# Kernel optimization log

Measured on AMD Instinct MI355X. Metric: run time of the kernel, lower is better.

## Reference

```python
import jax, jax.numpy as jnp
import numpy as np

TAU = 2.0
DECAY = float(np.exp(-1.0 / TAU))
THRESH = 1.0  # base_threshold; adaptive update only happens in training mode
LN_EPS = 1e-5
B, S, V, D, L = 16, 256, 32000, 512, 4  # d_state must equal d_model (see shape_source)

@jax.custom_vjp
def atan_spike(x):
    # spikingjelly surrogate.ATan: heaviside fwd, atan surrogate bwd (alpha=2)
    return (x >= 0).astype(x.dtype)

def _atan_fwd(x):
    return atan_spike(x), x

def _atan_bwd(x, g):
    alpha = 2.0
    s = (jnp.pi / 2.0) * alpha * x
    return (g * (alpha / 2.0) / (1.0 + s * s),)

atan_spike.defvjp(_atan_fwd, _atan_bwd)

def lif_step(mem, x):
    mem = mem * DECAY + x
    spike = atan_spike(mem - THRESH)
    mem = mem * (1.0 - jax.lax.stop_gradient(spike))  # reset uses spike.detach()
    return mem, spike

def layer_norm(x, g, b):
    m = jnp.mean(x, axis=-1, keepdims=True)
    v = jnp.mean(jnp.square(x - m), axis=-1, keepdims=True)
    return (x - m) / jnp.sqrt(v + LN_EPS) * g + b

def setup_inputs():
    key = jax.random.key(0)
    ks = jax.random.split(key, 8)
    s = 0.02
    return {
        'input_ids': jax.random.randint(ks[0], (B, S), 0, V),
        'embedding': jax.random.normal(ks[1], (V, D), jnp.float32) * s,
        'enc_W': jax.random.normal(ks[2], (D, D), jnp.float32) * s,
        'enc_b': jnp.zeros((D,), jnp.float32),
        'gen_W': jax.random.normal(ks[3], (L, D, D), jnp.float32) * s,
        'gen_b': jnp.zeros((L, D), jnp.float32),
        'inf_W': jax.random.normal(ks[4], (L, D, D), jnp.float32) * s,
        'inf_b': jnp.zeros((L, D), jnp.float32),
        'err_g': jnp.ones((L, D), jnp.float32),
        'err_b': jnp.zeros((L, D), jnp.float32),
        'st_g': jnp.ones((L, D), jnp.float32),
        'st_b': jnp.zeros((L, D), jnp.float32),
        'out_W': jax.random.normal(ks[5], (V, D), jnp.float32) * s,
        'out_b': jnp.zeros((V,), jnp.float32),
    }

def reference(input_ids, embedding, enc_W, enc_b, gen_W, gen_b, inf_W, inf_b, err_g, err_b, st_g, st_b, out_W, out_b):
    tok = embedding[input_ids]              # [B,S,D]
    xs = jnp.swapaxes(tok, 0, 1)            # [S,B,D] scan over time

    def pc_layer(j, gm, im, bottom_up, top_down):
        # PredictiveCodingLayer.forward (LIF mems gm/im are persistent state)
        gm, pred = lif_step(gm, top_down @ gen_W[j].T + gen_b[j])
        err = layer_norm(jax.nn.relu(bottom_up - pred), err_g[j], err_b[j])
        im, su = lif_step(im, err @ inf_W[j].T + inf_b[j])
        new_state = layer_norm(top_down + su, st_g[j], st_b[j])
        return gm, im, new_state, err, pred

    def step(carry, emb_t):
        enc_mem, gen_mem, inf_mem, states, spk, memp = carry
        enc_mem, bu = lif_step(enc_mem, emb_t @ enc_W.T + enc_b)
        # bottom-up pass
        for j in range(L):
            gm, im, st, err, _ = pc_layer(j, gen_mem[j], inf_mem[j], bu, states[j])
            gen_mem = gen_mem.at[j].set(gm)
            inf_mem = inf_mem.at[j].set(im)
            states = states.at[j].set(st)
            bu = jax.nn.relu(st)
            spk = spk + err.mean()
            memp = memp + jnp.abs(im).mean()
        # top-down generative pass (same layers called again: mems keep evolving)
        td = states[L - 1]
        zb = jnp.zeros_like(bu)
        for j in reversed(range(L)):
            gm, im, _, _, pred = pc_layer(j, gen_mem[j], inf_mem[j], zb, td)
            gen_mem = gen_mem.at[j].set(gm)
            inf_mem = inf_mem.at[j].set(im)
            td = pred
        logits = td @ out_W.T + out_b
        return (enc_mem, gen_mem, inf_mem, states, spk, memp), logits

    init = (jnp.zeros((B, D), jnp.float32), jnp.zeros((L, B, D), jnp.float32),
            jnp.zeros((L, B, D), jnp.float32), jnp.zeros((L, B, D), jnp.float32),
            jnp.float32(0.0), jnp.float32(0.0))
    (_, _, _, _, spk, memp), logits_sb = jax.lax.scan(step, init, xs)
    final_logits = jnp.swapaxes(logits_sb, 0, 1)  # [B,S,V]
    return final_logits, spk / S, memp / S
```

## Files before the change

kernel.cpp:

```cpp
#include <hip/hip_runtime.h>
#include <math.h>

#define S_ 256
#define B_ 16
#define D_ 512
#define V_ 32000
#define L_ 4
#define DEC_ 0.6065306597126334f

typedef short v8s __attribute__((ext_vector_type(8)));
typedef float v4f __attribute__((ext_vector_type(4)));

static __device__ __forceinline__ short f2bf(float f){
  union { float f; unsigned u; } v; v.f = f;
  unsigned r = (v.u + 0x7FFFu + ((v.u >> 16) & 1u)) >> 16;
  return (short)(unsigned short)r;
}

__global__ __launch_bounds__(64) void k_cj(const float* __restrict__ inf_W,
                                           const float* __restrict__ inf_b,
                                           const float* __restrict__ err_b,
                                           float* __restrict__ cvec,
                                           unsigned* __restrict__ counts,
                                           unsigned* __restrict__ bunz,
                                           float* __restrict__ accum){
  int g = blockIdx.x * 64 + threadIdx.x;
  #pragma unroll
  for (int i = 0; i < 2; ++i){
    counts[g + i*2048] = 0u;
    bunz[g + i*2048] = 0u;
  }
  if (g < 2) accum[g] = 0.0f;

  int j = blockIdx.x >> 3;
  int dp = (blockIdx.x & 7) * 64 + threadIdx.x;
  const float* row = inf_W + ((size_t)j * D_ + dp) * D_;
  const float* eb = err_b + j * D_;
  float acc = inf_b[j * D_ + dp];
  for (int d = 0; d < D_; d += 8){
    float4 w0 = *(const float4*)(row + d);
    float4 w1 = *(const float4*)(row + d + 4);
    float4 e0 = *(const float4*)(eb + d);
    float4 e1 = *(const float4*)(eb + d + 4);
    acc += e0.x*w0.x + e0.y*w0.y + e0.z*w0.z + e0.w*w0.w;
    acc += e1.x*w1.x + e1.y*w1.y + e1.z*w1.z + e1.w*w1.w;
  }
  cvec[j * D_ + dp] = acc;
}

__global__ __launch_bounds__(256) void k_gemm_enc(const int* __restrict__ ids,
                                                  const float* __restrict__ emb,
                                                  const float* __restrict__ encW,
                                                  const float* __restrict__ encb,
                                                  float* __restrict__ X){
  __shared__ __align__(16) short As[64*40];
  __shared__ __align__(16) short Bs[64*40];
  __shared__ int ids_s[64];
  const int t = threadIdx.x;
  const int bm = blockIdx.x, bn = blockIdx.y;
  if (t < 64){
    int mg = bm*64 + t;
    int s = mg >> 4, b = mg & 15;
    ids_s[t] = ids[b * S_ + s];
  }
  __syncthreads();
  const int arow = t >> 2;
  const int kc = (t & 3) * 8;
  const int wave = t >> 6;
  const int l = t & 63;
  const int lm = l & 15;
  const int q = l >> 4;
  v4f acc[4] = {};
  for (int k0 = 0; k0 < D_; k0 += 32){
    const float* asrc = emb + (size_t)ids_s[arow] * D_ + k0 + kc;
    float4 a0 = *(const float4*)asrc;
    float4 a1 = *(const float4*)(asrc + 4);
    const float* bsrc = encW + (size_t)(bn*64 + arow) * D_ + k0 + kc;
    float4 b0 = *(const float4*)bsrc;
    float4 b1 = *(const float4*)(bsrc + 4);
    v8s av, bv;
    av[0]=f2bf(a0.x); av[1]=f2bf(a0.y); av[2]=f2bf(a0.z); av[3]=f2bf(a0.w);
    av[4]=f2bf(a1.x); av[5]=f2bf(a1.y); av[6]=f2bf(a1.z); av[7]=f2bf(a1.w);
    bv[0]=f2bf(b0.x); bv[1]=f2bf(b0.y); bv[2]=f2bf(b0.z); bv[3]=f2bf(b0.w);
    bv[4]=f2bf(b1.x); bv[5]=f2bf(b1.y); bv[6]=f2bf(b1.z); bv[7]=f2bf(b1.w);
    *(v8s*)&As[arow*40 + kc] = av;
    *(v8s*)&Bs[arow*40 + kc] = bv;
    __syncthreads();
    v8s af = *(const v8s*)&As[(wave*16 + lm)*40 + q*8];
    #pragma unroll
    for (int n = 0; n < 4; ++n){
      v8s bf = *(const v8s*)&Bs[(n*16 + lm)*40 + q*8];
      acc[n] = __builtin_amdgcn_mfma_f32_16x16x32_bf16(af, bf, acc[n], 0, 0, 0);
    }
    __syncthreads();
  }
  #pragma unroll
  for (int n = 0; n < 4; ++n){
    #pragma unroll
    for (int i = 0; i < 4; ++i){
      int mloc = wave*16 + q*4 + i;
      int nloc = n*16 + lm;
      int r  = bm*64 + mloc;
      int nn = bn*64 + nloc;
      X[(size_t)r * D_ + nn] = acc[n][i] + encb[nn];
    }
  }
}

__global__ __launch_bounds__(64) void k_scan(const float* __restrict__ X,
                                             unsigned char* __restrict__ bu,
                                             unsigned* __restrict__ bunz){
  int g = blockIdx.x * 64 + threadIdx.x;
  int b = g >> 9;
  float mem = 0.0f;
  for (int s0 = 0; s0 < S_; s0 += 8){
    float x[8];
    #pragma unroll
    for (int i = 0; i < 8; ++i) x[i] = X[(size_t)(s0 + i) * (B_*D_) + g];
    #pragma unroll
    for (int i = 0; i < 8; ++i){
      mem = mem * DEC_ + x[i];
      float sp = (mem >= 1.0f) ? 1.0f : 0.0f;
      mem *= (1.0f - sp);
      bu[(size_t)(s0 + i) * (B_*D_) + g] = (unsigned char)sp;
      if (sp != 0.0f) atomicOr(&bunz[(s0 + i) * B_ + b], 1u);
    }
  }
}

__device__ __forceinline__ float wave_sum(float x){
  #pragma unroll
  for (int o = 32; o > 0; o >>= 1) x += __shfl_xor(x, o);
  return x;
}

__device__ void wave_matvec(const float* __restrict__ W, const float* __restrict__ bias,
                            const float x[8], float y[8], float* xs, int l){
  __syncthreads();
  #pragma unroll
  for (int i = 0; i < 8; ++i) xs[l + 64*i] = x[i];
  __syncthreads();
  #pragma unroll
  for (int i = 0; i < 8; ++i){
    int dp = l + 64*i;
    const float* row = W + (size_t)dp * D_;
    float acc = bias[dp];
    for (int d = 0; d < D_; d += 4){
      float4 w = *(const float4*)(row + d);
      acc += xs[d]*w.x + xs[d+1]*w.y + xs[d+2]*w.z + xs[d+3]*w.w;
    }
    y[i] = acc;
  }
}

__device__ void wave_ln(const float e[8], const float* __restrict__ g,
                        const float* __restrict__ bb, float out[8], int l){
  float s = 0.f;
  #pragma unroll
  for (int i = 0; i < 8; ++i) s += e[i];
  float m = wave_sum(s) * (1.0f/512.0f);
  float s2 = 0.f;
  #pragma unroll
  for (int i = 0; i < 8; ++i){ float d = e[i] - m; s2 += d*d; }
  float var = wave_sum(s2) * (1.0f/512.0f);
  float inv = 1.0f / sqrtf(var + 1e-5f);
  #pragma unroll
  for (int i = 0; i < 8; ++i){
    int d = l + 64*i;
    out[i] = (e[i] - m) * inv * g[d] + bb[d];
  }
}

__global__ __launch_bounds__(64) void k_sim(
    const float* __restrict__ gen_W, const float* __restrict__ gen_b,
    const float* __restrict__ inf_W, const float* __restrict__ inf_b,
    const float* __restrict__ err_g, const float* __restrict__ err_b,
    const float* __restrict__ st_g, const float* __restrict__ st_b,
    const unsigned char* __restrict__ bu8, const unsigned* __restrict__ bunz,
    const float* __restrict__ cvec,
    unsigned* __restrict__ counts, unsigned short* __restrict__ idxb,
    float* __restrict__ accum)
{
  const int b = blockIdx.x, l = threadIdx.x;
  __shared__ float xs[D_];
  __shared__ unsigned scnt;
  float st[4][8], gm[4][8], im[4][8];
  #pragma unroll
  for (int j = 0; j < 4; ++j)
    #pragma unroll
    for (int i = 0; i < 8; ++i){ st[j][i]=0.f; gm[j][i]=0.f; im[j][i]=0.f; }

  bool okz = true;
  #pragma unroll
  for (int j = 0; j < 4; ++j)
    #pragma unroll
    for (int i = 0; i < 8; ++i){
      int d = j*512 + l + 64*i;
      okz = okz && (gen_b[d]==0.f) && (inf_b[d]==0.f) && (err_b[d]==0.f) && (st_b[d]==0.f);
    }
  const bool bias_zero = (__all((int)okz) != 0);

  unsigned long long fl[4];
  #pragma unroll
  for (int w = 0; w < 4; ++w){
    unsigned v = bunz[(w*64 + l) * B_ + b];
    fl[w] = __ballot(v != 0u);
  }

  bool state_zero = true;
  float spk_acc = 0.f, memp_acc = 0.f;

  for (int t = 0; t < S_; ++t){
    bool nz = ((fl[t >> 6] >> (t & 63)) & 1ull) != 0ull;
    if (state_zero && bias_zero && !nz) continue;
    state_zero = false;

    float bu[8];
    #pragma unroll
    for (int i = 0; i < 8; ++i) bu[i] = (float)bu8[(size_t)(t*B_ + b)*D_ + l + 64*i];

    #pragma unroll
    for (int j = 0; j < 4; ++j){
      float y[8];
      wave_matvec(gen_W + (size_t)j*D_*D_, gen_b + j*D_, st[j], y, xs, l);
      float pred[8];
      #pragma unroll
      for (int i = 0; i < 8; ++i){
        gm[j][i] = gm[j][i]*DEC_ + y[i];
        pred[i] = (gm[j][i] >= 1.0f) ? 1.0f : 0.0f;
        gm[j][i] *= (1.0f - pred[i]);
      }
      float e[8];
      #pragma unroll
      for (int i = 0; i < 8; ++i){ float v = bu[i] - pred[i]; e[i] = v > 0.f ? v : 0.f; }
      float eo[8];
      wave_ln(e, err_g + j*D_, err_b + j*D_, eo, l);
      #pragma unroll
      for (int i = 0; i < 8; ++i) spk_acc += eo[i];
      float y2[8];
      wave_matvec(inf_W + (size_t)j*D_*D_, inf_b + j*D_, eo, y2, xs, l);
      float su[8];
      #pragma unroll
      for (int i = 0; i < 8; ++i){
        im[j][i] = im[j][i]*DEC_ + y2[i];
        su[i] = (im[j][i] >= 1.0f) ? 1.0f : 0.0f;
        im[j][i] *= (1.0f - su[i]);
        memp_acc += fabsf(im[j][i]);
      }
      float tmp[8];
      #pragma unroll
      for (int i = 0; i < 8; ++i) tmp[i] = st[j][i] + su[i];
      wave_ln(tmp, st_g + j*D_, st_b + j*D_, st[j], l);
      #pragma unroll
      for (int i = 0; i < 8; ++i) bu[i] = st[j][i] > 0.f ? st[j][i] : 0.f;
    }

    float td[8];
    #pragma unroll
    for (int i = 0; i < 8; ++i) td[i] = st[3][i];
    #pragma unroll
    for (int j = 3; j >= 0; --j){
      float y[8];
      wave_matvec(gen_W + (size_t)j*D_*D_, gen_b + j*D_, td, y, xs, l);
      #pragma unroll
      for (int i = 0; i < 8; ++i){
        gm[j][i] = gm[j][i]*DEC_ + y[i];
        float p = (gm[j][i] >= 1.0f) ? 1.0f : 0.0f;
        gm[j][i] *= (1.0f - p);
        td[i] = p;
      }
      #pragma unroll
      for (int i = 0; i < 8; ++i){
        float c = cvec[j*D_ + l + 64*i];
        im[j][i] = im[j][i]*DEC_ + c;
        float ss = (im[j][i] >= 1.0f) ? 1.0f : 0.0f;
        im[j][i] *= (1.0f - ss);
      }
    }

    if (l == 0) scnt = 0u;
    __syncthreads();
    unsigned base = (unsigned)(t*B_ + b) * D_;
    #pragma unroll
    for (int i = 0; i < 8; ++i){
      if (td[i] != 0.f){
        unsigned pos = atomicAdd(&scnt, 1u);
        idxb[base + pos] = (unsigned short)(l + 64*i);
      }
    }
    __syncthreads();
    if (l == 0) counts[t*B_ + b] = scnt;
  }
  spk_acc = wave_sum(spk_acc);
  memp_acc = wave_sum(memp_acc);
  if (l == 0){
    atomicAdd(&accum[0], spk_acc);
    atomicAdd(&accum[1], memp_acc);
  }
}

__global__ __launch_bounds__(256) void k_logits(const unsigned* __restrict__ counts,
                                                const unsigned short* __restrict__ idxb,
                                                const float* __restrict__ outW,
                                                const float* __restrict__ outb,
                                                const float* __restrict__ accum,
                                                float* __restrict__ out){
  __shared__ unsigned short sidx[D_];
  int bs = blockIdx.x;
  int b = bs >> 8, s = bs & 255;
  if (bs == 0 && threadIdx.x == 0){
    const float inv = 1.0f / (float)(B_ * D_ * S_);
    out[(size_t)B_ * S_ * V_ + 0] = accum[0] * inv;
    out[(size_t)B_ * S_ * V_ + 1] = accum[1] * inv;
  }
  unsigned k = counts[s * B_ + b];
  const float4* ob4 = (const float4*)outb;
  float4* o4 = (float4*)(out + (size_t)bs * V_);
  if (k == 0){
    #pragma unroll 4
    for (int v4 = threadIdx.x; v4 < V_/4; v4 += 256) o4[v4] = ob4[v4];
  } else {
    unsigned base = (unsigned)(s * B_ + b) * D_;
    for (unsigned i = threadIdx.x; i < k; i += 256) sidx[i] = idxb[base + i];
    __syncthreads();
    for (int v4 = threadIdx.x; v4 < V_/4; v4 += 256){
      float4 a = ob4[v4];
      int v = v4 * 4;
      for (unsigned i = 0; i < k; ++i){
        int d = sidx[i];
        a.x += outW[(size_t)(v+0)*D_ + d];
        a.y += outW[(size_t)(v+1)*D_ + d];
        a.z += outW[(size_t)(v+2)*D_ + d];
        a.w += outW[(size_t)(v+3)*D_ + d];
      }
      o4[v4] = a;
    }
  }
}

extern "C" void kernel_launch(void* const* d_in, const int* in_sizes, int n_in,
                              void* d_out, int out_size, void* d_ws, size_t ws_size,
                              hipStream_t stream){
  (void)in_sizes; (void)n_in; (void)out_size; (void)ws_size;
  const int*   input_ids = (const int*)d_in[0];
  const float* embedding = (const float*)d_in[1];
  const float* enc_W = (const float*)d_in[2];
  const float* enc_b = (const float*)d_in[3];
  const float* gen_W = (const float*)d_in[4];
  const float* gen_b = (const float*)d_in[5];
  const float* inf_W = (const float*)d_in[6];
  const float* inf_b = (const float*)d_in[7];
  const float* err_g = (const float*)d_in[8];
  const float* err_b = (const float*)d_in[9];
  const float* st_g  = (const float*)d_in[10];
  const float* st_b  = (const float*)d_in[11];
  const float* out_W = (const float*)d_in[12];
  const float* out_b = (const float*)d_in[13];
  float* out = (float*)d_out;
  char* ws = (char*)d_ws;

  float*          X      = (float*)(ws + 0);
  unsigned char*  bu     = (unsigned char*)(ws + 8388608);
  unsigned short* idxb   = (unsigned short*)(ws + 10485760);
  unsigned*       counts = (unsigned*)(ws + 14680064);
  unsigned*       bunz   = (unsigned*)(ws + 14696448);
  float*          cvec   = (float*)(ws + 14712832);
  float*          accum  = (float*)(ws + 14721024);

  hipLaunchKernelGGL(k_cj, dim3(32), dim3(64), 0, stream,
                     inf_W, inf_b, err_b, cvec, counts, bunz, accum);
  hipLaunchKernelGGL(k_gemm_enc, dim3(64, 8), dim3(256), 0, stream,
                     input_ids, embedding, enc_W, enc_b, X);
  hipLaunchKernelGGL(k_scan, dim3(128), dim3(64), 0, stream, X, bu, bunz);
  hipLaunchKernelGGL(k_sim, dim3(16), dim3(64), 0, stream,
                     gen_W, gen_b, inf_W, inf_b, err_g, err_b, st_g, st_b,
                     bu, bunz, cvec, counts, idxb, accum);
  hipLaunchKernelGGL(k_logits, dim3(4096), dim3(256), 0, stream,
                     counts, idxb, out_W, out_b, accum, out);
}
```

Baseline: 710.9 us.

## Fold prep kernel into encoder/scan and retile logits with nontemporal stores

```diff
diff --git a/kernel.cpp b/kernel.cpp
--- a/kernel.cpp
+++ b/kernel.cpp
@@ -17,47 +17,25 @@
   return (short)(unsigned short)r;
 }
 
-__global__ __launch_bounds__(64) void k_cj(const float* __restrict__ inf_W,
-                                           const float* __restrict__ inf_b,
-                                           const float* __restrict__ err_b,
-                                           float* __restrict__ cvec,
-                                           unsigned* __restrict__ counts,
-                                           unsigned* __restrict__ bunz,
-                                           float* __restrict__ accum){
-  int g = blockIdx.x * 64 + threadIdx.x;
-  #pragma unroll
-  for (int i = 0; i < 2; ++i){
-    counts[g + i*2048] = 0u;
-    bunz[g + i*2048] = 0u;
-  }
-  if (g < 2) accum[g] = 0.0f;
-
-  int j = blockIdx.x >> 3;
-  int dp = (blockIdx.x & 7) * 64 + threadIdx.x;
-  const float* row = inf_W + ((size_t)j * D_ + dp) * D_;
-  const float* eb = err_b + j * D_;
-  float acc = inf_b[j * D_ + dp];
-  for (int d = 0; d < D_; d += 8){
-    float4 w0 = *(const float4*)(row + d);
-    float4 w1 = *(const float4*)(row + d + 4);
-    float4 e0 = *(const float4*)(eb + d);
-    float4 e1 = *(const float4*)(eb + d + 4);
-    acc += e0.x*w0.x + e0.y*w0.y + e0.z*w0.z + e0.w*w0.w;
-    acc += e1.x*w1.x + e1.y*w1.y + e1.z*w1.z + e1.w*w1.w;
-  }
-  cvec[j * D_ + dp] = acc;
-}
-
 __global__ __launch_bounds__(256) void k_gemm_enc(const int* __restrict__ ids,
                                                   const float* __restrict__ emb,
                                                   const float* __restrict__ encW,
                                                   const float* __restrict__ encb,
-                                                  float* __restrict__ X){
+                                                  float* __restrict__ X,
+                                                  unsigned* __restrict__ counts,
+                                                  unsigned* __restrict__ bunz,
+                                                  float* __restrict__ accum){
   __shared__ __align__(16) short As[64*40];
   __shared__ __align__(16) short Bs[64*40];
   __shared__ int ids_s[64];
   const int t = threadIdx.x;
   const int bm = blockIdx.x, bn = blockIdx.y;
+  if (bn == 0 && bm < 16){
+    int g = bm*256 + t;
+    counts[g] = 0u;
+    bunz[g] = 0u;
+    if (g < 2) accum[g] = 0.0f;
+  }
   if (t < 64){
     int mg = bm*64 + t;
     int s = mg >> 4, b = mg & 15;
@@ -109,8 +87,31 @@
 
 __global__ __launch_bounds__(64) void k_scan(const float* __restrict__ X,
                                              unsigned char* __restrict__ bu,
-                                             unsigned* __restrict__ bunz){
-  int g = blockIdx.x * 64 + threadIdx.x;
+                                             unsigned* __restrict__ bunz,
+                                             const float* __restrict__ inf_W,
+                                             const float* __restrict__ inf_b,
+                                             const float* __restrict__ err_b,
+                                             float* __restrict__ cvec){
+  int bx = blockIdx.x;
+  if (bx >= 128){
+    int r = bx - 128;
+    int j = r >> 3;
+    int dp = (r & 7) * 64 + threadIdx.x;
+    const float* row = inf_W + ((size_t)j * D_ + dp) * D_;
+    const float* eb = err_b + j * D_;
+    float acc = inf_b[j * D_ + dp];
+    for (int d = 0; d < D_; d += 8){
+      float4 w0 = *(const float4*)(row + d);
+      float4 w1 = *(const float4*)(row + d + 4);
+      float4 e0 = *(const float4*)(eb + d);
+      float4 e1 = *(const float4*)(eb + d + 4);
+      acc += e0.x*w0.x + e0.y*w0.y + e0.z*w0.z + e0.w*w0.w;
+      acc += e1.x*w1.x + e1.y*w1.y + e1.z*w1.z + e1.w*w1.w;
+    }
+    cvec[j * D_ + dp] = acc;
+    return;
+  }
+  int g = bx * 64 + threadIdx.x;
   int b = g >> 9;
   float mem = 0.0f;
   for (int s0 = 0; s0 < S_; s0 += 8){
@@ -299,41 +300,57 @@
   }
 }
 
-__global__ __launch_bounds__(256) void k_logits(const unsigned* __restrict__ counts,
-                                                const unsigned short* __restrict__ idxb,
-                                                const float* __restrict__ outW,
-                                                const float* __restrict__ outb,
-                                                const float* __restrict__ accum,
-                                                float* __restrict__ out){
-  __shared__ unsigned short sidx[D_];
-  int bs = blockIdx.x;
-  int b = bs >> 8, s = bs & 255;
-  if (bs == 0 && threadIdx.x == 0){
+__global__ __launch_bounds__(64) void k_logits(const unsigned* __restrict__ counts,
+                                               const unsigned short* __restrict__ idxb,
+                                               const float* __restrict__ outW,
+                                               const float* __restrict__ outb,
+                                               const float* __restrict__ accum,
+                                               float* __restrict__ out){
+  const int chunk = blockIdx.x % 25;
+  const int rg = blockIdx.x / 25;
+  const int lane = threadIdx.x;
+  if (blockIdx.x == 0 && lane == 0){
     const float inv = 1.0f / (float)(B_ * D_ * S_);
     out[(size_t)B_ * S_ * V_ + 0] = accum[0] * inv;
     out[(size_t)B_ * S_ * V_ + 1] = accum[1] * inv;
   }
-  unsigned k = counts[s * B_ + b];
-  const float4* ob4 = (const float4*)outb;
-  float4* o4 = (float4*)(out + (size_t)bs * V_);
-  if (k == 0){
-    #pragma unroll 4
-    for (int v4 = threadIdx.x; v4 < V_/4; v4 += 256) o4[v4] = ob4[v4];
-  } else {
-    unsigned base = (unsigned)(s * B_ + b) * D_;
-    for (unsigned i = threadIdx.x; i < k; i += 256) sidx[i] = idxb[base + i];
-    __syncthreads();
-    for (int v4 = threadIdx.x; v4 < V_/4; v4 += 256){
-      float4 a = ob4[v4];
-      int v = v4 * 4;
-      for (unsigned i = 0; i < k; ++i){
-        int d = sidx[i];
-        a.x += outW[(size_t)(v+0)*D_ + d];
-        a.y += outW[(size_t)(v+1)*D_ + d];
-        a.z += outW[(size_t)(v+2)*D_ + d];
-        a.w += outW[(size_t)(v+3)*D_ + d];
-      }
-      o4[v4] = a;
+  const int colbase = chunk * 1280;
+  v4f pay[5];
+  #pragma unroll
+  for (int k = 0; k < 5; ++k)
+    pay[k] = *(const v4f*)(outb + colbase + k*256 + lane*4);
+
+  int prow = rg*32 + (lane & 31);
+  unsigned myc = counts[(prow & 255) * B_ + (prow >> 8)];
+
+  for (int r = 0; r < 32; ++r){
+    int row = rg*32 + r;
+    unsigned cnt = (unsigned)__shfl((int)myc, r);
+    float* dst = out + (size_t)row * V_ + colbase;
+    if (cnt == 0){
+      #pragma unroll
+      for (int k = 0; k < 5; ++k)
+        __builtin_nontemporal_store(pay[k], (v4f*)(dst + k*256 + lane*4));
+    } else {
+      int s = row & 255, b = row >> 8;
+      unsigned base = (unsigned)(s * B_ + b) * D_;
+      v4f acc[5];
+      #pragma unroll
+      for (int k = 0; k < 5; ++k) acc[k] = pay[k];
+      for (unsigned i = 0; i < cnt; ++i){
+        int d = idxb[base + i];
+        #pragma unroll
+        for (int k = 0; k < 5; ++k){
+          int v = colbase + k*256 + lane*4;
+          acc[k].x += outW[(size_t)(v+0)*D_ + d];
+          acc[k].y += outW[(size_t)(v+1)*D_ + d];
+          acc[k].z += outW[(size_t)(v+2)*D_ + d];
+          acc[k].w += outW[(size_t)(v+3)*D_ + d];
+        }
+      }
+      #pragma unroll
+      for (int k = 0; k < 5; ++k)
+        __builtin_nontemporal_store(acc[k], (v4f*)(dst + k*256 + lane*4));
     }
   }
 }
@@ -367,14 +384,13 @@
   float*          cvec   = (float*)(ws + 14712832);
   float*          accum  = (float*)(ws + 14721024);
 
-  hipLaunchKernelGGL(k_cj, dim3(32), dim3(64), 0, stream,
-                     inf_W, inf_b, err_b, cvec, counts, bunz, accum);
   hipLaunchKernelGGL(k_gemm_enc, dim3(64, 8), dim3(256), 0, stream,
-                     input_ids, embedding, enc_W, enc_b, X);
-  hipLaunchKernelGGL(k_scan, dim3(128), dim3(64), 0, stream, X, bu, bunz);
+                     input_ids, embedding, enc_W, enc_b, X, counts, bunz, accum);
+  hipLaunchKernelGGL(k_scan, dim3(160), dim3(64), 0, stream,
+                     X, bu, bunz, inf_W, inf_b, err_b, cvec);
   hipLaunchKernelGGL(k_sim, dim3(16), dim3(64), 0, stream,
                      gen_W, gen_b, inf_W, inf_b, err_g, err_b, st_g, st_b,
                      bu, bunz, cvec, counts, idxb, accum);
-  hipLaunchKernelGGL(k_logits, dim3(4096), dim3(256), 0, stream,
+  hipLaunchKernelGGL(k_logits, dim3(3200), dim3(64), 0, stream,
                      counts, idxb, out_W, out_b, accum, out);
 }
```

Result: no change. 704.4 us (-0.9%).
